# Kernel optimization log

Hardware: AMD Instinct MI355X
Metric: run time of the kernel (lower is better)

Reference implementation:

```python
import jax, jax.numpy as jnp
import numpy as np

N_NODES = 30000
N_EDGES = 480000
F_IN = 64
F_EDGE = 16
HID = 128
N_LAYERS = 3
N_CLASSES = 10
MSG_EPS = 1e-7   # GENConv eps added after ReLU
SM_EPS = 1e-16   # PyG softmax denom eps
LN_EPS = 1e-5


def _layer_norm(x, g, b):
    m = jnp.mean(x, axis=-1, keepdims=True)
    v = jnp.mean((x - m) ** 2, axis=-1, keepdims=True)
    return (x - m) * jax.lax.rsqrt(v + LN_EPS) * g + b


def _gen_conv(h, ea, src, dst, t, w1, b1, lg, lb, w2, b2):
    # GENConv message: relu(x_j + e_ij) + eps  -> [E, H]
    msg = jax.nn.relu(h[src] + ea) + MSG_EPS
    # learnable-temperature segment softmax over incoming edges of each node
    logits = msg * t
    mx = jax.ops.segment_max(logits, dst, num_segments=N_NODES)
    e = jnp.exp(logits - mx[dst])
    s = jax.ops.segment_sum(e, dst, num_segments=N_NODES)
    alpha = e / (s[dst] + SM_EPS)
    agg = jax.ops.segment_sum(msg * alpha, dst, num_segments=N_NODES)  # [N, H]
    # out = MLP(aggr + x): Linear(H,2H) -> LayerNorm -> ReLU -> Linear(2H,H)
    z = agg + h
    z = jax.nn.relu(_layer_norm(z @ w1 + b1, lg, lb)) @ w2 + b2
    return z


def setup_inputs() -> dict:
    key = jax.random.key(0)
    ks = jax.random.split(key, 10)
    g = lambda k, s, sc=0.05: jax.random.normal(k, s, jnp.float32) * sc
    return {
        "x": g(ks[0], (N_NODES, F_IN), 1.0),
        "edge_attr": g(ks[1], (N_EDGES, F_EDGE), 1.0),
        "node_enc_w": g(ks[2], (F_IN, HID)),
        "node_enc_b": jnp.zeros((HID,), jnp.float32),
        "edge_enc_w": g(ks[3], (F_EDGE, HID)),
        "edge_enc_b": jnp.zeros((HID,), jnp.float32),
        "mlp1_w": g(ks[4], (N_LAYERS, HID, 2 * HID)),
        "mlp1_b": jnp.zeros((N_LAYERS, 2 * HID), jnp.float32),
        "mlp_ln_g": jnp.ones((N_LAYERS, 2 * HID), jnp.float32),
        "mlp_ln_b": jnp.zeros((N_LAYERS, 2 * HID), jnp.float32),
        "mlp2_w": g(ks[5], (N_LAYERS, 2 * HID, HID)),
        "mlp2_b": jnp.zeros((N_LAYERS, HID), jnp.float32),
        "t": jnp.ones((N_LAYERS,), jnp.float32),
        "norm_g": jnp.ones((N_LAYERS, HID), jnp.float32),
        "norm_b": jnp.zeros((N_LAYERS, HID), jnp.float32),
        "lin_w": g(ks[6], (HID, N_CLASSES)),
        "lin_b": jnp.zeros((N_CLASSES,), jnp.float32),
        "edge_index": jax.random.randint(ks[7], (2, N_EDGES), 0, N_NODES, jnp.int32),
    }


def reference(x, edge_attr, node_enc_w, node_enc_b, edge_enc_w, edge_enc_b,
              mlp1_w, mlp1_b, mlp_ln_g, mlp_ln_b, mlp2_w, mlp2_b, t,
              norm_g, norm_b, lin_w, lin_b, edge_index):
    src, dst = edge_index[0], edge_index[1]
    ea = edge_attr @ edge_enc_w + edge_enc_b   # [E, H]
    h = x @ node_enc_w + node_enc_b            # [N, H]
    # first layer applies the conv directly (as in the original forward)
    h = _gen_conv(h, ea, src, dst, t[0], mlp1_w[0], mlp1_b[0],
                  mlp_ln_g[0], mlp_ln_b[0], mlp2_w[0], mlp2_b[0])
    # remaining DeepGCN res+ layers: h = h + conv(dropout(relu(norm(h))))
    for i in range(1, N_LAYERS):
        res = h
        z = jax.nn.relu(_layer_norm(h, norm_g[i], norm_b[i]))  # dropout p=0.1 -> identity in eval
        z = _gen_conv(z, ea, src, dst, t[i], mlp1_w[i], mlp1_b[i],
                      mlp_ln_g[i], mlp_ln_b[i], mlp2_w[i], mlp2_b[i])
        h = z + res
    # final norm/act from layers[0] then classifier (dropout -> identity in eval)
    h = jax.nn.relu(_layer_norm(h, norm_g[0], norm_b[0]))
    return h @ lin_w + lin_b
```

## Files before the change

### kernel.cpp

```cpp
#include <hip/hip_runtime.h>
#include <hip/hip_bf16.h>

#define NN 30000
#define NE 480000
#define NROWT 1875

typedef __attribute__((ext_vector_type(8))) short short8;
typedef __attribute__((ext_vector_type(4))) float floatx4;

__device__ __forceinline__ short f2bs(float f) {
    __hip_bfloat16 h = __float2bfloat16(f);
    return *reinterpret_cast<short*>(&h);
}

__device__ __forceinline__ short2 split_bf16(float f) {
    __hip_bfloat16 h = __float2bfloat16(f);
    float r = f - __bfloat162float(h);
    __hip_bfloat16 l = __float2bfloat16(r);
    short2 out;
    out.x = *reinterpret_cast<short*>(&h);
    out.y = *reinterpret_cast<short*>(&l);
    return out;
}

__global__ void presplit_all(const float* __restrict__ ew, const float* __restrict__ nw,
                             const float* __restrict__ m1w, const float* __restrict__ m2w,
                             const float* __restrict__ lw,
                             short* __restrict__ ew_h, short* __restrict__ ew_l,
                             short* __restrict__ nw_h, short* __restrict__ nw_l,
                             short* __restrict__ m1_h, short* __restrict__ m1_l,
                             short* __restrict__ m2_h, short* __restrict__ m2_l,
                             short* __restrict__ lw_h, short* __restrict__ lw_l)
{
    int i = blockIdx.x * 256 + threadIdx.x;
    if (i < 2048) {
        int k = i >> 7, n = i & 127;
        short2 s = split_bf16(ew[i]);
        ew_h[n * 16 + k] = s.x; ew_l[n * 16 + k] = s.y;
    } else if (i < 10240) {
        int j = i - 2048;
        int k = j >> 7, n = j & 127;
        short2 s = split_bf16(nw[j]);
        nw_h[n * 64 + k] = s.x; nw_l[n * 64 + k] = s.y;
    } else if (i < 108544) {
        int j = i - 10240;
        int l = j >> 15, jj = j & 32767;
        int k = jj >> 8, n = jj & 255;
        short2 s = split_bf16(m1w[j]);
        m1_h[(size_t)l * 32768 + n * 128 + k] = s.x;
        m1_l[(size_t)l * 32768 + n * 128 + k] = s.y;
    } else if (i < 206848) {
        int j = i - 108544;
        int l = j >> 15, jj = j & 32767;
        int k = jj >> 7, n = jj & 127;
        short2 s = split_bf16(m2w[j]);
        m2_h[(size_t)l * 32768 + n * 256 + k] = s.x;
        m2_l[(size_t)l * 32768 + n * 256 + k] = s.y;
    } else if (i < 208896) {
        int j = i - 206848;
        int k = j >> 4, n = j & 15;
        short2 s = (n < 10) ? split_bf16(lw[k * 10 + n]) : short2{0, 0};
        lw_h[n * 128 + k] = s.x; lw_l[n * 128 + k] = s.y;
    }
}

template<int K, int N>
__launch_bounds__(256)
__global__ void gemm_a32(const float* __restrict__ A, const short* __restrict__ Bh,
                         const short* __restrict__ Bl, const float* __restrict__ bias,
                         float* __restrict__ C, unsigned* __restrict__ hp, int total_waves)
{
    int wave = ((blockIdx.x * 256) + threadIdx.x) >> 6;
    if (wave >= total_waves) return;
    constexpr int NT = N / 16;
    const int mt = wave / NT, nt = wave % NT;
    const int lane = threadIdx.x & 63;
    const int l15 = lane & 15, quad = lane >> 4;
    const int row = mt * 16 + l15;
    const int col = nt * 16 + l15;
    floatx4 acc = {0.f, 0.f, 0.f, 0.f};
#pragma unroll
    for (int k0 = 0; k0 < K; k0 += 32) {
        const int kb = k0 + quad * 8;
        short8 ah, al;
        const float* ap = A + (size_t)row * K + kb;
        floatx4 a0 = *(const floatx4*)ap;
        floatx4 a1 = *(const floatx4*)(ap + 4);
#pragma unroll
        for (int j = 0; j < 4; j++) {
            short2 s0 = split_bf16(a0[j]); ah[j] = s0.x; al[j] = s0.y;
            short2 s1 = split_bf16(a1[j]); ah[j + 4] = s1.x; al[j + 4] = s1.y;
        }
        short8 bh = *(const short8*)(Bh + (size_t)col * K + kb);
        short8 bl = *(const short8*)(Bl + (size_t)col * K + kb);
        acc = __builtin_amdgcn_mfma_f32_16x16x32_bf16(ah, bh, acc, 0, 0, 0);
        acc = __builtin_amdgcn_mfma_f32_16x16x32_bf16(al, bh, acc, 0, 0, 0);
        acc = __builtin_amdgcn_mfma_f32_16x16x32_bf16(ah, bl, acc, 0, 0, 0);
    }
    float bv = bias[col];
#pragma unroll
    for (int r = 0; r < 4; r++) {
        int ro = mt * 16 + quad * 4 + r;
        float v = acc[r] + bv;
        C[(size_t)ro * N + col] = v;
        int mb = (int)(unsigned short)f2bs(v);
        int ob = __shfl_xor(mb, 1, 64);
        if ((l15 & 1) == 0)
            hp[(size_t)ro * 64 + nt * 8 + (l15 >> 1)] = (unsigned)mb | ((unsigned)ob << 16);
    }
}

template<int K, int NTOT, int NTW, int NREAL>
__launch_bounds__(256)
__global__ void gemm_s(const short* __restrict__ Ah, const short* __restrict__ Al,
                       const short* __restrict__ Bh, const short* __restrict__ Bl,
                       const float* __restrict__ bias, float* __restrict__ C, int total_waves)
{
    int wave = ((blockIdx.x * 256) + threadIdx.x) >> 6;
    if (wave >= total_waves) return;
    constexpr int NG = NTOT / (16 * NTW);
    const int mt = wave / NG, g = wave % NG;
    const int lane = threadIdx.x & 63;
    const int l15 = lane & 15, quad = lane >> 4;
    const int row = mt * 16 + l15;
    floatx4 acc[NTW];
#pragma unroll
    for (int t = 0; t < NTW; t++) acc[t] = {0.f, 0.f, 0.f, 0.f};
#pragma unroll
    for (int k0 = 0; k0 < K; k0 += 32) {
        const int kb = k0 + quad * 8;
        short8 ah = *(const short8*)(Ah + (size_t)row * K + kb);
        short8 al = *(const short8*)(Al + (size_t)row * K + kb);
#pragma unroll
        for (int t = 0; t < NTW; t++) {
            int col = g * NTW * 16 + t * 16 + l15;
            short8 bh = *(const short8*)(Bh + (size_t)col * K + kb);
            short8 bl = *(const short8*)(Bl + (size_t)col * K + kb);
            acc[t] = __builtin_amdgcn_mfma_f32_16x16x32_bf16(ah, bh, acc[t], 0, 0, 0);
            acc[t] = __builtin_amdgcn_mfma_f32_16x16x32_bf16(al, bh, acc[t], 0, 0, 0);
            acc[t] = __builtin_amdgcn_mfma_f32_16x16x32_bf16(ah, bl, acc[t], 0, 0, 0);
        }
    }
#pragma unroll
    for (int t = 0; t < NTW; t++) {
        int col = g * NTW * 16 + t * 16 + l15;
        if (col < NREAL) {
            float bv = bias[col];
#pragma unroll
            for (int r = 0; r < 4; r++) {
                int ro = mt * 16 + quad * 4 + r;
                C[(size_t)ro * NREAL + col] = acc[t][r] + bv;
            }
        }
    }
}

__launch_bounds__(256)
__global__ void gemm_ea(const float* __restrict__ edge_attr, const int* __restrict__ eidx_csr,
                        const short* __restrict__ Bh, const short* __restrict__ Bl,
                        const float* __restrict__ bias, unsigned* __restrict__ ea4)
{
    __shared__ short tile[2][16][132];
    const int wv = threadIdx.x >> 6;
    const int sub = wv >> 1, g = wv & 1;
    const int lane = threadIdx.x & 63;
    const int l15 = lane & 15, quad = lane >> 4;
    const int p = blockIdx.x * 32 + sub * 16 + l15;
    short8 a;
    if (quad < 2) {
        int e = eidx_csr[p];
        const float* ap = edge_attr + (size_t)e * 16 + quad * 8;
        floatx4 a0 = *(const floatx4*)ap;
        floatx4 a1 = *(const floatx4*)(ap + 4);
#pragma unroll
        for (int j = 0; j < 4; j++) { a[j] = f2bs(a0[j]); a[j + 4] = f2bs(a1[j]); }
    } else {
#pragma unroll
        for (int j = 0; j < 8; j++) a[j] = 0;
    }
    floatx4 acc[4];
#pragma unroll
    for (int t = 0; t < 4; t++) acc[t] = {0.f, 0.f, 0.f, 0.f};
#pragma unroll
    for (int t = 0; t < 4; t++) {
        int col = g * 64 + t * 16 + l15;
        short8 bh, bl;
        if (quad < 2) {
            bh = *(const short8*)(Bh + (size_t)col * 16 + quad * 8);
            bl = *(const short8*)(Bl + (size_t)col * 16 + quad * 8);
        } else {
#pragma unroll
            for (int j = 0; j < 8; j++) { bh[j] = 0; bl[j] = 0; }
        }
        acc[t] = __builtin_amdgcn_mfma_f32_16x16x32_bf16(a, bh, acc[t], 0, 0, 0);
        acc[t] = __builtin_amdgcn_mfma_f32_16x16x32_bf16(a, bl, acc[t], 0, 0, 0);
    }
#pragma unroll
    for (int t = 0; t < 4; t++) {
        int col = g * 64 + t * 16 + l15;
        float bv = bias[col];
#pragma unroll
        for (int r = 0; r < 4; r++)
            tile[sub][quad * 4 + r][col] = f2bs(acc[t][r] + bv);
    }
    __syncthreads();
#pragma unroll
    for (int c = 0; c < 2; c++) {
        int idx = threadIdx.x + 256 * c;
        int o = idx * 16;
        int g4l = o >> 10;
        int lp = (o & 1023) >> 4;
        unsigned u[4];
#pragma unroll
        for (int e = 0; e < 4; e++) {
            int rl = g4l * 4 + e;
            u[e] = *(const unsigned*)&tile[rl >> 4][rl & 15][2 * lp];
        }
        uint4 val = make_uint4(u[0], u[1], u[2], u[3]);
        *(uint4*)((char*)ea4 + (size_t)blockIdx.x * 8192 + o) = val;
    }
}

__global__ void zero_kernel(int* __restrict__ p, int n)
{
    int i = blockIdx.x * 256 + threadIdx.x;
    if (i < n) p[i] = 0;
}

__global__ void hist_kernel(const int* __restrict__ dst, int* __restrict__ count)
{
    int e = blockIdx.x * 256 + threadIdx.x;
    if (e < NE) atomicAdd(count + dst[e], 1);
}

__launch_bounds__(1024)
__global__ void scan_kernel(const int* __restrict__ count, int* __restrict__ rowptr)
{
    __shared__ int part[1024];
    const int t = threadIdx.x;
    const int CH = (NN + 1023) / 1024;
    const int base = t * CH;
    int sum = 0;
    for (int j = 0; j < CH; j++) {
        int idx = base + j;
        if (idx < NN) sum += count[idx];
    }
    part[t] = sum;
    __syncthreads();
    for (int d = 1; d < 1024; d <<= 1) {
        int v = (t >= d) ? part[t - d] : 0;
        __syncthreads();
        part[t] += v;
        __syncthreads();
    }
    int off = (t == 0) ? 0 : part[t - 1];
    for (int j = 0; j < CH; j++) {
        int idx = base + j;
        if (idx < NN) { rowptr[idx] = off; off += count[idx]; }
    }
    if (t == 1023) rowptr[NN] = part[1023];
}

__global__ void scatter_kernel(const int* __restrict__ src, const int* __restrict__ dst,
                               const int* __restrict__ rowptr, int* __restrict__ cursor,
                               int* __restrict__ src_csr, int* __restrict__ eidx_csr)
{
    int e = blockIdx.x * 256 + threadIdx.x;
    if (e >= NE) return;
    int d = dst[e];
    int pos = rowptr[d] + atomicAdd(cursor + d, 1);
    src_csr[pos] = src[e];
    eidx_csr[pos] = e;
}

__device__ __forceinline__ void updm(float hv, float av, float tt, float m,
                                     float& s, float& n)
{
    float g = fmaxf(hv + av, 0.f) + 1e-7f;
    float e = __expf(g * tt) * m;
    s += e;
    n = fmaf(g, e, n);
}

__launch_bounds__(256)
__global__ void agg_kernel(const unsigned* __restrict__ hp, const float* __restrict__ hres,
                           const uint4* __restrict__ ea4q, const int* __restrict__ src_csr,
                           const int* __restrict__ rowptr, const float* __restrict__ tptr,
                           int layer, unsigned* __restrict__ Zp)
{
    __shared__ float4 part[4][64];
    const int wv = threadIdx.x >> 6;
    const int node = blockIdx.x * 2 + (wv >> 1);
    const int par = wv & 1;
    const int lane = threadIdx.x & 63;
    const float tt = tptr[layer];
    const int start = rowptr[node];
    const int end = rowptr[node + 1];
    const int g0 = start >> 2, g1 = (end + 3) >> 2;
    float s0a = 0.f, s1a = 0.f, n0a = 0.f, n1a = 0.f;
    float s0b = 0.f, s1b = 0.f, n0b = 0.f, n1b = 0.f;

#define PROC(GG, S0, S1, N0, N1)                                                   \
    {                                                                              \
        uint4 uu = ea4q[((size_t)(GG) << 6) + lane];                               \
        int4 sv = *(const int4*)(src_csr + 4 * (GG));                              \
        int jb = 4 * (GG);                                                         \
        float m0 = (jb     >= start && jb     < end) ? 1.f : 0.f;                  \
        float m1 = (jb + 1 >= start && jb + 1 < end) ? 1.f : 0.f;                  \
        float m2 = (jb + 2 >= start && jb + 2 < end) ? 1.f : 0.f;                  \
        float m3 = (jb + 3 >= start && jb + 3 < end) ? 1.f : 0.f;                  \
        unsigned ha = hp[(size_t)sv.x * 64 + lane];                                \
        unsigned hb = hp[(size_t)sv.y * 64 + lane];                                \
        unsigned hc = hp[(size_t)sv.z * 64 + lane];                                \
        unsigned hd = hp[(size_t)sv.w * 64 + lane];                                \
        updm(__uint_as_float(ha << 16), __uint_as_float(uu.x << 16), tt, m0, S0, N0); \
        updm(__uint_as_float(ha & 0xffff0000u), __uint_as_float(uu.x & 0xffff0000u), tt, m0, S1, N1); \
        updm(__uint_as_float(hb << 16), __uint_as_float(uu.y << 16), tt, m1, S0, N0); \
        updm(__uint_as_float(hb & 0xffff0000u), __uint_as_float(uu.y & 0xffff0000u), tt, m1, S1, N1); \
        updm(__uint_as_float(hc << 16), __uint_as_float(uu.z << 16), tt, m2, S0, N0); \
        updm(__uint_as_float(hc & 0xffff0000u), __uint_as_float(uu.z & 0xffff0000u), tt, m2, S1, N1); \
        updm(__uint_as_float(hd << 16), __uint_as_float(uu.w << 16), tt, m3, S0, N0); \
        updm(__uint_as_float(hd & 0xffff0000u), __uint_as_float(uu.w & 0xffff0000u), tt, m3, S1, N1); \
    }

    int g = g0 + par;
    for (; g + 2 < g1; g += 4) {
        PROC(g, s0a, s1a, n0a, n1a);
        PROC(g + 2, s0b, s1b, n0b, n1b);
    }
    if (g < g1) PROC(g, s0a, s1a, n0a, n1a);
#undef PROC
    float ps0 = s0a + s0b, ps1 = s1a + s1b, pn0 = n0a + n0b, pn1 = n1a + n1b;
    part[wv][lane] = make_float4(ps0, ps1, pn0, pn1);
    __syncthreads();
    if (par == 0) {
        float4 o = part[wv + 1][lane];
        float s0 = ps0 + o.x, s1 = ps1 + o.y;
        float n0 = pn0 + o.z, n1 = pn1 + o.w;
        float2 res = ((const float2*)hres)[(size_t)node * 64 + lane];
        float ox = n0 / (s0 + 1e-16f) + res.x;
        float oy = n1 / (s1 + 1e-16f) + res.y;
        Zp[(size_t)node * 64 + lane] =
            (unsigned)(unsigned short)f2bs(ox) | ((unsigned)(unsigned short)f2bs(oy) << 16);
    }
}

template<bool HAS_RES, bool FINAL>
__launch_bounds__(256)
__global__ void mlp_fused(const short* __restrict__ Ap,
                          const short* __restrict__ B1h, const short* __restrict__ B1l,
                          const float* __restrict__ b1, const float* __restrict__ g1,
                          const float* __restrict__ be1,
                          const short* __restrict__ B2h, const short* __restrict__ B2l,
                          const float* __restrict__ b2, const float* __restrict__ res,
                          const float* __restrict__ g2, const float* __restrict__ be2,
                          short* __restrict__ z1h,
                          float* __restrict__ Hout, float* __restrict__ HinOut,
                          unsigned* __restrict__ HP,
                          short* __restrict__ Fh, short* __restrict__ Fl)
{
    __shared__ __align__(16) short lds[32768];
    const int wv = threadIdx.x >> 6;
    const int lane = threadIdx.x & 63;
    const int l15 = lane & 15, quad = lane >> 4;
    const int tile = blockIdx.x * 4 + wv;
    const bool valid = (tile < NROWT);
    const int row = tile * 16 + l15;

    floatx4 acc[16];
#pragma unroll
    for (int t = 0; t < 16; t++) acc[t] = {0.f, 0.f, 0.f, 0.f};
    for (int hf = 0; hf < 2; hf++) {
        __syncthreads();
        {
            const float4* s1p = (const float4*)(B1h + hf * 16384);
            const float4* s2p = (const float4*)(B1l + hf * 16384);
            float4* d = (float4*)lds;
#pragma unroll
            for (int i = 0; i < 8; i++) {
                int t8 = threadIdx.x + 256 * i;
                int col = t8 >> 4, k8 = t8 & 15;
                int unit = col * 16 + (k8 ^ (col & 15));
                d[unit] = s1p[t8];
                d[2048 + unit] = s2p[t8];
            }
        }
        __syncthreads();
        if (valid) {
#pragma unroll
            for (int k0 = 0; k0 < 128; k0 += 32) {
                const int kb = k0 + quad * 8;
                const int kb8 = kb >> 3;
                short8 ah = *(const short8*)(Ap + (size_t)row * 128 + kb);
#pragma unroll
                for (int t = 0; t < 8; t++) {
                    int col = t * 16 + l15;
                    int unit = col * 16 + (kb8 ^ (col & 15));
                    const short* bp = lds + unit * 8;
                    short8 bh = *(const short8*)bp;
                    short8 bl = *(const short8*)(bp + 16384);
                    int ti = hf * 8 + t;
                    acc[ti] = __builtin_amdgcn_mfma_f32_16x16x32_bf16(ah, bh, acc[ti], 0, 0, 0);
                    acc[ti] = __builtin_amdgcn_mfma_f32_16x16x32_bf16(ah, bl, acc[ti], 0, 0, 0);
                }
            }
        }
    }
    if (valid) {
#pragma unroll
        for (int t = 0; t < 16; t++) {
            float bv = b1[t * 16 + l15];
#pragma unroll
            for (int r = 0; r < 4; r++) acc[t][r] += bv;
        }
        float s1[4] = {0.f, 0.f, 0.f, 0.f}, s2[4] = {0.f, 0.f, 0.f, 0.f};
#pragma unroll
        for (int t = 0; t < 16; t++)
#pragma unroll
            for (int r = 0; r < 4; r++) { s1[r] += acc[t][r]; s2[r] += acc[t][r] * acc[t][r]; }
#pragma unroll
        for (int m = 1; m <= 8; m <<= 1)
#pragma unroll
            for (int r = 0; r < 4; r++) {
                s1[r] += __shfl_xor(s1[r], m, 64);
                s2[r] += __shfl_xor(s2[r], m, 64);
            }
        float mean[4], rstd[4];
#pragma unroll
        for (int r = 0; r < 4; r++) {
            mean[r] = s1[r] * (1.f / 256.f);
            float var = s2[r] * (1.f / 256.f) - mean[r] * mean[r];
            rstd[r] = rsqrtf(var + 1e-5f);
        }
#pragma unroll
        for (int t = 0; t < 16; t++) {
            int col = t * 16 + l15;
            float gg = g1[col], bb = be1[col];
#pragma unroll
            for (int r = 0; r < 4; r++) {
                float y = fmaxf((acc[t][r] - mean[r]) * rstd[r] * gg + bb, 0.f);
                int ro = tile * 16 + quad * 4 + r;
                z1h[(size_t)ro * 256 + col] = f2bs(y);
            }
        }
    }
    floatx4 acc2[8];
#pragma unroll
    for (int t = 0; t < 8; t++) acc2[t] = {0.f, 0.f, 0.f, 0.f};
    for (int hf = 0; hf < 2; hf++) {
        __syncthreads();
        {
            const float4* s1p = (const float4*)(B2h + hf * 16384);
            const float4* s2p = (const float4*)(B2l + hf * 16384);
            float4* d = (float4*)lds;
#pragma unroll
            for (int i = 0; i < 8; i++) {
                int t8 = threadIdx.x + 256 * i;
                int col = t8 >> 5, k8 = t8 & 31;
                int unit = col * 32 + (k8 ^ (col & 15));
                d[unit] = s1p[t8];
                d[2048 + unit] = s2p[t8];
            }
        }
        __syncthreads();
        if (valid) {
#pragma unroll
            for (int k0 = 0; k0 < 256; k0 += 32) {
                const int kb = k0 + quad * 8;
                const int kb8 = kb >> 3;
                short8 zh = *(const short8*)(z1h + (size_t)row * 256 + kb);
#pragma unroll
                for (int t = 0; t < 4; t++) {
                    int col = t * 16 + l15;
                    int unit = col * 32 + (kb8 ^ (col & 15));
                    const short* bp = lds + unit * 8;
                    short8 bh = *(const short8*)bp;
                    short8 bl = *(const short8*)(bp + 16384);
                    int ti = hf * 4 + t;
                    acc2[ti] = __builtin_amdgcn_mfma_f32_16x16x32_bf16(zh, bh, acc2[ti], 0, 0, 0);
                    acc2[ti] = __builtin_amdgcn_mfma_f32_16x16x32_bf16(zh, bl, acc2[ti], 0, 0, 0);
                }
            }
        }
    }
    if (valid) {
#pragma unroll
        for (int t = 0; t < 8; t++) {
            int col = t * 16 + l15;
            float bv = b2[col];
#pragma unroll
            for (int r = 0; r < 4; r++) {
                acc2[t][r] += bv;
                if (HAS_RES) {
                    int ro = tile * 16 + quad * 4 + r;
                    acc2[t][r] += res[(size_t)ro * 128 + col];
                }
            }
        }
        float s1[4] = {0.f, 0.f, 0.f, 0.f}, s2[4] = {0.f, 0.f, 0.f, 0.f};
#pragma unroll
        for (int t = 0; t < 8; t++)
#pragma unroll
            for (int r = 0; r < 4; r++) { s1[r] += acc2[t][r]; s2[r] += acc2[t][r] * acc2[t][r]; }
#pragma unroll
        for (int m = 1; m <= 8; m <<= 1)
#pragma unroll
            for (int r = 0; r < 4; r++) {
                s1[r] += __shfl_xor(s1[r], m, 64);
                s2[r] += __shfl_xor(s2[r], m, 64);
            }
        float mean[4], rstd[4];
#pragma unroll
        for (int r = 0; r < 4; r++) {
            mean[r] = s1[r] * (1.f / 128.f);
            float var = s2[r] * (1.f / 128.f) - mean[r] * mean[r];
            rstd[r] = rsqrtf(var + 1e-5f);
        }
#pragma unroll
        for (int t = 0; t < 8; t++) {
            int col = t * 16 + l15;
            float gg = g2[col], bb = be2[col];
#pragma unroll
            for (int r = 0; r < 4; r++) {
                int ro = tile * 16 + quad * 4 + r;
                float x = acc2[t][r];
                float y = fmaxf((x - mean[r]) * rstd[r] * gg + bb, 0.f);
                if (FINAL) {
                    short2 sp = split_bf16(y);
                    Fh[(size_t)ro * 128 + col] = sp.x;
                    Fl[(size_t)ro * 128 + col] = sp.y;
                } else {
                    Hout[(size_t)ro * 128 + col] = x;
                    HinOut[(size_t)ro * 128 + col] = y;
                    int yb = (int)(unsigned short)f2bs(y);
                    int ob = __shfl_xor(yb, 1, 64);
                    if ((l15 & 1) == 0)
                        HP[(size_t)ro * 64 + t * 8 + (l15 >> 1)] =
                            (unsigned)yb | ((unsigned)ob << 16);
                }
            }
        }
    }
}

extern "C" void kernel_launch(void* const* d_in, const int* in_sizes, int n_in,
                              void* d_out, int out_size, void* d_ws, size_t ws_size,
                              hipStream_t stream)
{
    const float* x         = (const float*)d_in[0];
    const float* edge_attr = (const float*)d_in[1];
    const float* nw        = (const float*)d_in[2];
    const float* nb        = (const float*)d_in[3];
    const float* ew        = (const float*)d_in[4];
    const float* eb        = (const float*)d_in[5];
    const float* m1w       = (const float*)d_in[6];
    const float* m1b       = (const float*)d_in[7];
    const float* lng       = (const float*)d_in[8];
    const float* lnb       = (const float*)d_in[9];
    const float* m2w       = (const float*)d_in[10];
    const float* m2b       = (const float*)d_in[11];
    const float* tpr       = (const float*)d_in[12];
    const float* ng        = (const float*)d_in[13];
    const float* nbb       = (const float*)d_in[14];
    const float* lw        = (const float*)d_in[15];
    const float* lb        = (const float*)d_in[16];
    const int* ei  = (const int*)d_in[17];
    const int* src = ei;
    const int* dst = ei + NE;

    char* w = (char*)d_ws;
    unsigned* ea4 = (unsigned*)w; w += (size_t)NE * 128 * 2;
    int* src_csr  = (int*)w; w += (size_t)NE * 4;
    int* eidx_csr = (int*)w; w += (size_t)NE * 4;
    unsigned* hp  = (unsigned*)w; w += (size_t)NN * 64 * 4;
    unsigned* zp  = (unsigned*)w; w += (size_t)NN * 64 * 4;
    float* h   = (float*)w; w += (size_t)NN * 128 * 4;
    float* hin = (float*)w; w += (size_t)NN * 128 * 4;
    short* fin_h  = (short*)w; w += (size_t)NN * 128 * 2;
    short* fin_l  = (short*)w; w += (size_t)NN * 128 * 2;
    short* z1s_h  = (short*)w; w += (size_t)NN * 256 * 2;
    short* ew_h = (short*)w; w += (size_t)128 * 16 * 2;
    short* ew_l = (short*)w; w += (size_t)128 * 16 * 2;
    short* nw_h = (short*)w; w += (size_t)128 * 64 * 2;
    short* nw_l = (short*)w; w += (size_t)128 * 64 * 2;
    short* m1_h = (short*)w; w += (size_t)3 * 256 * 128 * 2;
    short* m1_l = (short*)w; w += (size_t)3 * 256 * 128 * 2;
    short* m2_h = (short*)w; w += (size_t)3 * 128 * 256 * 2;
    short* m2_l = (short*)w; w += (size_t)3 * 128 * 256 * 2;
    short* lw_h = (short*)w; w += (size_t)16 * 128 * 2;
    short* lw_l = (short*)w; w += (size_t)16 * 128 * 2;
    int* count  = (int*)w;   w += (size_t)NN * 4;
    int* cursor = (int*)w;   w += (size_t)NN * 4;
    int* rowptr = (int*)w;   w += (size_t)(NN + 1) * 4;

    zero_kernel<<<(2 * NN + 255) / 256, 256, 0, stream>>>(count, 2 * NN);
    hist_kernel<<<(NE + 255) / 256, 256, 0, stream>>>(dst, count);
    scan_kernel<<<1, 1024, 0, stream>>>(count, rowptr);
    scatter_kernel<<<(NE + 255) / 256, 256, 0, stream>>>(src, dst, rowptr, cursor,
                                                         src_csr, eidx_csr);

    presplit_all<<<(208896 + 255) / 256, 256, 0, stream>>>(
        ew, nw, m1w, m2w, lw, ew_h, ew_l, nw_h, nw_l, m1_h, m1_l, m2_h, m2_l, lw_h, lw_l);

    gemm_ea<<<NE / 32, 256, 0, stream>>>(edge_attr, eidx_csr, ew_h, ew_l, eb, ea4);
    gemm_a32<64, 128><<<(NN / 16) * 8 / 4, 256, 0, stream>>>(x, nw_h, nw_l, nb, h, hp,
                                                             (NN / 16) * 8);

    const uint4* ea4q = (const uint4*)ea4;
    const int mgrid = (NROWT + 3) / 4;
    for (int layer = 0; layer < 3; ++layer) {
        const float* hi = (layer == 0) ? h : hin;
        agg_kernel<<<NN / 2, 256, 0, stream>>>(hp, hi, ea4q, src_csr, rowptr, tpr, layer, zp);
        if (layer == 0) {
            mlp_fused<false, false><<<mgrid, 256, 0, stream>>>(
                (const short*)zp, m1_h, m1_l, m1b, lng, lnb,
                m2_h, m2_l, m2b, nullptr, ng + 128, nbb + 128,
                z1s_h, h, hin, hp, nullptr, nullptr);
        } else if (layer == 1) {
            mlp_fused<true, false><<<mgrid, 256, 0, stream>>>(
                (const short*)zp, m1_h + 32768, m1_l + 32768, m1b + 256, lng + 256, lnb + 256,
                m2_h + 32768, m2_l + 32768, m2b + 128, h, ng + 256, nbb + 256,
                z1s_h, h, hin, hp, nullptr, nullptr);
        } else {
            mlp_fused<true, true><<<mgrid, 256, 0, stream>>>(
                (const short*)zp, m1_h + 65536, m1_l + 65536, m1b + 512, lng + 512, lnb + 512,
                m2_h + 65536, m2_l + 65536, m2b + 256, h, ng, nbb,
                z1s_h, nullptr, nullptr, nullptr, fin_h, fin_l);
        }
    }
    gemm_s<128, 16, 1, 10><<<((NN / 16) + 3) / 4, 256, 0, stream>>>(
        fin_h, fin_l, lw_h, lw_l, lb, (float*)d_out, NN / 16);
}
```

Before: 478.3 us.

## Fuse final classifier into last MLP kernel and read residual from bf16 buffer

```diff
diff --git a/kernel.cpp b/kernel.cpp
--- a/kernel.cpp
+++ b/kernel.cpp
@@ -110,51 +110,6 @@
     }
 }
 
-template<int K, int NTOT, int NTW, int NREAL>
-__launch_bounds__(256)
-__global__ void gemm_s(const short* __restrict__ Ah, const short* __restrict__ Al,
-                       const short* __restrict__ Bh, const short* __restrict__ Bl,
-                       const float* __restrict__ bias, float* __restrict__ C, int total_waves)
-{
-    int wave = ((blockIdx.x * 256) + threadIdx.x) >> 6;
-    if (wave >= total_waves) return;
-    constexpr int NG = NTOT / (16 * NTW);
-    const int mt = wave / NG, g = wave % NG;
-    const int lane = threadIdx.x & 63;
-    const int l15 = lane & 15, quad = lane >> 4;
-    const int row = mt * 16 + l15;
-    floatx4 acc[NTW];
-#pragma unroll
-    for (int t = 0; t < NTW; t++) acc[t] = {0.f, 0.f, 0.f, 0.f};
-#pragma unroll
-    for (int k0 = 0; k0 < K; k0 += 32) {
-        const int kb = k0 + quad * 8;
-        short8 ah = *(const short8*)(Ah + (size_t)row * K + kb);
-        short8 al = *(const short8*)(Al + (size_t)row * K + kb);
-#pragma unroll
-        for (int t = 0; t < NTW; t++) {
-            int col = g * NTW * 16 + t * 16 + l15;
-            short8 bh = *(const short8*)(Bh + (size_t)col * K + kb);
-            short8 bl = *(const short8*)(Bl + (size_t)col * K + kb);
-            acc[t] = __builtin_amdgcn_mfma_f32_16x16x32_bf16(ah, bh, acc[t], 0, 0, 0);
-            acc[t] = __builtin_amdgcn_mfma_f32_16x16x32_bf16(al, bh, acc[t], 0, 0, 0);
-            acc[t] = __builtin_amdgcn_mfma_f32_16x16x32_bf16(ah, bl, acc[t], 0, 0, 0);
-        }
-    }
-#pragma unroll
-    for (int t = 0; t < NTW; t++) {
-        int col = g * NTW * 16 + t * 16 + l15;
-        if (col < NREAL) {
-            float bv = bias[col];
-#pragma unroll
-            for (int r = 0; r < 4; r++) {
-                int ro = mt * 16 + quad * 4 + r;
-                C[(size_t)ro * NREAL + col] = acc[t][r] + bv;
-            }
-        }
-    }
-}
-
 __launch_bounds__(256)
 __global__ void gemm_ea(const float* __restrict__ edge_attr, const int* __restrict__ eidx_csr,
                         const short* __restrict__ Bh, const short* __restrict__ Bl,
@@ -283,7 +238,7 @@
 }
 
 __launch_bounds__(256)
-__global__ void agg_kernel(const unsigned* __restrict__ hp, const float* __restrict__ hres,
+__global__ void agg_kernel(const unsigned* __restrict__ hp,
                            const uint4* __restrict__ ea4q, const int* __restrict__ src_csr,
                            const int* __restrict__ rowptr, const float* __restrict__ tptr,
                            int layer, unsigned* __restrict__ Zp)
@@ -337,9 +292,9 @@
         float4 o = part[wv + 1][lane];
         float s0 = ps0 + o.x, s1 = ps1 + o.y;
         float n0 = pn0 + o.z, n1 = pn1 + o.w;
-        float2 res = ((const float2*)hres)[(size_t)node * 64 + lane];
-        float ox = n0 / (s0 + 1e-16f) + res.x;
-        float oy = n1 / (s1 + 1e-16f) + res.y;
+        unsigned ur = hp[(size_t)node * 64 + lane];
+        float ox = n0 / (s0 + 1e-16f) + __uint_as_float(ur << 16);
+        float oy = n1 / (s1 + 1e-16f) + __uint_as_float(ur & 0xffff0000u);
         Zp[(size_t)node * 64 + lane] =
             (unsigned)(unsigned short)f2bs(ox) | ((unsigned)(unsigned short)f2bs(oy) << 16);
     }
@@ -355,9 +310,9 @@
                           const float* __restrict__ b2, const float* __restrict__ res,
                           const float* __restrict__ g2, const float* __restrict__ be2,
                           short* __restrict__ z1h,
-                          float* __restrict__ Hout, float* __restrict__ HinOut,
-                          unsigned* __restrict__ HP,
-                          short* __restrict__ Fh, short* __restrict__ Fl)
+                          float* __restrict__ Hout, unsigned* __restrict__ HP,
+                          const short* __restrict__ lwh, const short* __restrict__ lwl,
+                          const float* __restrict__ lb, float* __restrict__ Dout)
 {
     __shared__ __align__(16) short lds[32768];
     const int wv = threadIdx.x >> 6;
@@ -483,6 +438,9 @@
             }
         }
     }
+    if (FINAL) __syncthreads();
+    short* yh = lds + wv * 2176;
+    short* yl = lds + 8704 + wv * 2176;
     if (valid) {
 #pragma unroll
         for (int t = 0; t < 8; t++) {
@@ -527,17 +485,38 @@
                 float y = fmaxf((x - mean[r]) * rstd[r] * gg + bb, 0.f);
                 if (FINAL) {
                     short2 sp = split_bf16(y);
-                    Fh[(size_t)ro * 128 + col] = sp.x;
-                    Fl[(size_t)ro * 128 + col] = sp.y;
+                    yh[(quad * 4 + r) * 136 + col] = sp.x;
+                    yl[(quad * 4 + r) * 136 + col] = sp.y;
                 } else {
                     Hout[(size_t)ro * 128 + col] = x;
-                    HinOut[(size_t)ro * 128 + col] = y;
                     int yb = (int)(unsigned short)f2bs(y);
                     int ob = __shfl_xor(yb, 1, 64);
                     if ((l15 & 1) == 0)
                         HP[(size_t)ro * 64 + t * 8 + (l15 >> 1)] =
                             (unsigned)yb | ((unsigned)ob << 16);
                 }
+            }
+        }
+    }
+    if (FINAL && valid) {
+        floatx4 accc = {0.f, 0.f, 0.f, 0.f};
+#pragma unroll
+        for (int k0 = 0; k0 < 128; k0 += 32) {
+            const int kb = k0 + quad * 8;
+            short8 ah = *(const short8*)(yh + l15 * 136 + kb);
+            short8 al = *(const short8*)(yl + l15 * 136 + kb);
+            short8 bh = *(const short8*)(lwh + l15 * 128 + kb);
+            short8 bl = *(const short8*)(lwl + l15 * 128 + kb);
+            accc = __builtin_amdgcn_mfma_f32_16x16x32_bf16(ah, bh, accc, 0, 0, 0);
+            accc = __builtin_amdgcn_mfma_f32_16x16x32_bf16(al, bh, accc, 0, 0, 0);
+            accc = __builtin_amdgcn_mfma_f32_16x16x32_bf16(ah, bl, accc, 0, 0, 0);
+        }
+        if (l15 < 10) {
+            float bv = lb[l15];
+#pragma unroll
+            for (int r = 0; r < 4; r++) {
+                int ro = tile * 16 + quad * 4 + r;
+                Dout[(size_t)ro * 10 + l15] = accc[r] + bv;
             }
         }
     }
@@ -575,9 +554,6 @@
     unsigned* hp  = (unsigned*)w; w += (size_t)NN * 64 * 4;
     unsigned* zp  = (unsigned*)w; w += (size_t)NN * 64 * 4;
     float* h   = (float*)w; w += (size_t)NN * 128 * 4;
-    float* hin = (float*)w; w += (size_t)NN * 128 * 4;
-    short* fin_h  = (short*)w; w += (size_t)NN * 128 * 2;
-    short* fin_l  = (short*)w; w += (size_t)NN * 128 * 2;
     short* z1s_h  = (short*)w; w += (size_t)NN * 256 * 2;
     short* ew_h = (short*)w; w += (size_t)128 * 16 * 2;
     short* ew_l = (short*)w; w += (size_t)128 * 16 * 2;
@@ -609,25 +585,22 @@
     const uint4* ea4q = (const uint4*)ea4;
     const int mgrid = (NROWT + 3) / 4;
     for (int layer = 0; layer < 3; ++layer) {
-        const float* hi = (layer == 0) ? h : hin;
-        agg_kernel<<<NN / 2, 256, 0, stream>>>(hp, hi, ea4q, src_csr, rowptr, tpr, layer, zp);
+        agg_kernel<<<NN / 2, 256, 0, stream>>>(hp, ea4q, src_csr, rowptr, tpr, layer, zp);
         if (layer == 0) {
             mlp_fused<false, false><<<mgrid, 256, 0, stream>>>(
                 (const short*)zp, m1_h, m1_l, m1b, lng, lnb,
                 m2_h, m2_l, m2b, nullptr, ng + 128, nbb + 128,
-                z1s_h, h, hin, hp, nullptr, nullptr);
+                z1s_h, h, hp, nullptr, nullptr, nullptr, nullptr);
         } else if (layer == 1) {
             mlp_fused<true, false><<<mgrid, 256, 0, stream>>>(
                 (const short*)zp, m1_h + 32768, m1_l + 32768, m1b + 256, lng + 256, lnb + 256,
                 m2_h + 32768, m2_l + 32768, m2b + 128, h, ng + 256, nbb + 256,
-                z1s_h, h, hin, hp, nullptr, nullptr);
+                z1s_h, h, hp, nullptr, nullptr, nullptr, nullptr);
         } else {
             mlp_fused<true, true><<<mgrid, 256, 0, stream>>>(
                 (const short*)zp, m1_h + 65536, m1_l + 65536, m1b + 512, lng + 512, lnb + 512,
                 m2_h + 65536, m2_l + 65536, m2b + 256, h, ng, nbb,
-                z1s_h, nullptr, nullptr, nullptr, fin_h, fin_l);
-        }
-    }
-    gemm_s<128, 16, 1, 10><<<((NN / 16) + 3) / 4, 256, 0, stream>>>(
-        fin_h, fin_l, lw_h, lw_l, lb, (float*)d_out, NN / 16);
-}
+                z1s_h, nullptr, nullptr, lw_h, lw_l, lb, (float*)d_out);
+        }
+    }
+}
```

After: 455.1 us. 1.05x faster.
